# Kernel tuning notes

Hardware: AMD Instinct MI355X
Metric: run time of the kernel (lower is better)

Reference implementation:

```python
import jax, jax.numpy as jnp
import numpy as np

N, E, D, ED = 10000, 50000, 32, 16
DIMS = [(D, 8 * D), (8 * D, 16 * D), (16 * D, 16 * D), (16 * D, 16 * D)]
BI_OUT = 8 * D + ED  # 272


def _gat(h, src, dst, ea, Wl, Wr, We, att, b, n):
    """GATv2Conv, heads=1: score = att . leaky_relu(Wl x_j + Wr x_i + We e_ij); msg = Wl x_j."""
    xl = h @ Wl
    xr = h @ Wr
    ee = ea @ We
    s = jax.nn.leaky_relu(xl[src] + xr[dst] + ee, 0.2)   # [E_aug, out]
    alpha = s @ att                                       # [E_aug]
    amax = jax.lax.stop_gradient(jax.ops.segment_max(alpha, dst, num_segments=n))
    ex = jnp.exp(alpha - amax[dst])
    den = jax.ops.segment_sum(ex, dst, num_segments=n)
    w = ex / jnp.maximum(den[dst], 1e-16)
    return jax.ops.segment_sum(xl[src] * w[:, None], dst, num_segments=n) + b


def _forward(x, edge_attr, Wl0, Wr0, We0, a0, b0, Wl1, Wr1, We1, a1, b1,
             Wl2, Wr2, We2, a2, b2, Wl3, Wr3, We3, a3, b3,
             Wbi, bbi, Wm1, bm1, Wm2, bm2, Wm3, bm3, edge_index):
    src, dst = edge_index[0], edge_index[1]
    # self loops with edge_attr fill_value='mean' (mean of incoming edge_attr per target node)
    cnt = jax.ops.segment_sum(jnp.ones((E,), jnp.float32), dst, num_segments=N)
    mean_attr = jax.ops.segment_sum(edge_attr, dst, num_segments=N) / jnp.maximum(cnt, 1.0)[:, None]
    loop = jnp.arange(N, dtype=edge_index.dtype)
    src_a = jnp.concatenate([src, loop])
    dst_a = jnp.concatenate([dst, loop])
    ea_a = jnp.concatenate([edge_attr, mean_attr], axis=0)

    h = x
    layers = [(Wl0, Wr0, We0, a0, b0), (Wl1, Wr1, We1, a1, b1),
              (Wl2, Wr2, We2, a2, b2), (Wl3, Wr3, We3, a3, b3)]
    for i, (Wl, Wr, We, a, b) in enumerate(layers):
        h = _gat(h, src_a, dst_a, ea_a, Wl, Wr, We, a, b, N)
        if i < 3:
            h = jax.nn.relu(h)

    # edge scoring: gather both endpoints, bilinear with edge_attr, then MLP -> sigmoid
    z = jnp.concatenate([h[src], h[dst]], axis=1)           # [E, 2*16*D] = [E, 1024]
    bi = jnp.einsum('ni,kij,nj->nk', z, Wbi, edge_attr) + bbi  # [E, 272]
    m = jax.nn.relu(bi @ Wm1 + bm1)
    m = jax.nn.relu(m @ Wm2 + bm2)
    return jax.nn.sigmoid(m @ Wm3 + bm3)                    # [E, 1]


def setup_inputs() -> dict:
    ki = iter(jax.random.split(jax.random.key(0), 40))

    def rn(shape, s=0.05):
        return jax.random.normal(next(ki), shape, dtype=jnp.float32) * s

    inp = {
        "x": rn((N, D), 1.0),
        "edge_attr": rn((E, ED), 1.0),
        "edge_index": jax.random.randint(next(ki), (2, E), 0, N, dtype=jnp.int32),
    }
    for i, (din, dout) in enumerate(DIMS):
        inp[f"Wl{i}"] = rn((din, dout))
        inp[f"Wr{i}"] = rn((din, dout))
        inp[f"We{i}"] = rn((ED, dout))
        inp[f"a{i}"] = rn((dout,))
        inp[f"b{i}"] = jnp.zeros((dout,), jnp.float32)
    inp["Wbi"] = rn((BI_OUT, 2 * 16 * D, ED), 0.02)
    inp["bbi"] = jnp.zeros((BI_OUT,), jnp.float32)
    inp["Wm1"] = rn((BI_OUT, BI_OUT))
    inp["bm1"] = jnp.zeros((BI_OUT,), jnp.float32)
    inp["Wm2"] = rn((BI_OUT, D))
    inp["bm2"] = jnp.zeros((D,), jnp.float32)
    inp["Wm3"] = rn((D, 1))
    inp["bm3"] = jnp.zeros((1,), jnp.float32)
    return inp


def reference(x, edge_attr, edge_index, Wl0, Wr0, We0, a0, b0, Wl1, Wr1, We1, a1, b1,
              Wl2, Wr2, We2, a2, b2, Wl3, Wr3, We3, a3, b3,
              Wbi, bbi, Wm1, bm1, Wm2, bm2, Wm3, bm3):
    return _forward(x, edge_attr, Wl0, Wr0, We0, a0, b0, Wl1, Wr1, We1, a1, b1,
                    Wl2, Wr2, We2, a2, b2, Wl3, Wr3, We3, a3, b3,
                    Wbi, bbi, Wm1, bm1, Wm2, bm2, Wm3, bm3, edge_index)
```

## Files before the change

### kernel.cpp

```cpp
#include <hip/hip_runtime.h>
#include <hip/hip_bf16.h>
#include <hip/hip_fp16.h>
#include <cstdio>

#define N_NODES 10000
#define M_NODEP 10240
#define N_EDGES 50000
#define M_EDGEP 50176
#define E_AUG   60000
#define E_AUGP  60160
#define ED      16
#define BI_OUT  272
#define KP      288

typedef __attribute__((ext_vector_type(8))) short s16x8;
typedef __attribute__((ext_vector_type(4))) short s16x4;
typedef __attribute__((ext_vector_type(8))) _Float16 h16x8;
typedef __attribute__((ext_vector_type(4))) _Float16 h16x4;
typedef __attribute__((ext_vector_type(4))) float f32x4;

__device__ inline void stc(float* p, float v){ *p = v; }
__device__ inline void stc(__hip_bfloat16* p, float v){ *p = __float2bfloat16(v); }
__device__ inline void stc(__half* p, float v){ *p = __float2half(v); }
__device__ inline float bf2f(short s){ return __uint_as_float(((unsigned)(unsigned short)s) << 16); }
__device__ inline short f2bf(float f){ __hip_bfloat16 h = __float2bfloat16(f); return *(short*)&h; }

__device__ __forceinline__ void gl2lds16(const void* g, void* l){
  __builtin_amdgcn_global_load_lds((const __attribute__((address_space(1))) void*)g,
                                   (__attribute__((address_space(3))) void*)l, 16, 0, 0);
}

__global__ void edge_attr_sum_k(const float* __restrict__ ea, const int* __restrict__ ei,
                                float* __restrict__ meanat, float* __restrict__ cntF){
  int t = blockIdx.x*256 + threadIdx.x;
  if (t >= N_EDGES*ED) return;
  int e = t >> 4, j = t & 15;
  int dst = ei[N_EDGES + e];
  atomicAdd(&meanat[dst*ED + j], ea[t]);
  if (j == 0) atomicAdd(&cntF[dst], 1.0f);
}

__global__ void mean_div_k(float* __restrict__ meanat, const float* __restrict__ cntF){
  int t = blockIdx.x*256 + threadIdx.x;
  if (t >= N_NODES*ED) return;
  meanat[t] /= fmaxf(cntF[t>>4], 1.0f);
}

__global__ void scan_k(const float* __restrict__ cntF, int* __restrict__ rowptr){
  __shared__ int s[1024];
  int tid = threadIdx.x;
  int loc[10]; int sum = 0;
  #pragma unroll
  for (int k = 0; k < 10; ++k){
    int i = tid*10 + k;
    int v = (i < N_NODES) ? ((int)cntF[i] + 1) : 0;
    loc[k] = sum; sum += v;
  }
  s[tid] = sum; __syncthreads();
  for (int off = 1; off < 1024; off <<= 1){
    int t2 = (tid >= off) ? s[tid-off] : 0;
    __syncthreads();
    s[tid] += t2;
    __syncthreads();
  }
  int pre = s[tid] - sum;
  #pragma unroll
  for (int k = 0; k < 10; ++k){
    int i = tid*10 + k;
    if (i < N_NODES) rowptr[i] = pre + loc[k];
  }
  if (tid == 1023) rowptr[N_NODES] = s[1023];
}

__global__ void scatter_k(const int* __restrict__ ei, const int* __restrict__ rowptr,
                          int* __restrict__ fill, int* __restrict__ csr){
  int e = blockIdx.x*256 + threadIdx.x;
  if (e >= E_AUG) return;
  int dst = (e < N_EDGES) ? ei[N_EDGES+e] : (e - N_EDGES);
  int pos = rowptr[dst] + atomicAdd(&fill[dst], 1);
  csr[pos] = e;
}

template<typename TC, bool BIAS, bool RELU>
__global__ __launch_bounds__(256)
void mfma_gemm_k(const __hip_bfloat16* __restrict__ A, const __hip_bfloat16* __restrict__ Bt,
                 TC* __restrict__ C, const float* __restrict__ bias,
                 int Mstore, int K, int lda, int ldb, int ldc){
  __shared__ __align__(16) __hip_bfloat16 Asm[4096];
  __shared__ __align__(16) __hip_bfloat16 Bsm[4096];
  const int tid = threadIdx.x;
  const int lane = tid & 63, wave = tid >> 6;
  const int wm = (wave >> 1) * 64, wn = (wave & 1) * 64;
  const int m0 = blockIdx.x * 128, n0 = blockIdx.y * 128;
  const int quad = lane >> 4, r16 = lane & 15;

  f32x4 acc[4][4];
  #pragma unroll
  for (int i = 0; i < 4; ++i)
    #pragma unroll
    for (int j = 0; j < 4; ++j)
      acc[i][j] = (f32x4){0.f, 0.f, 0.f, 0.f};

  const int rl = lane >> 2, cq = lane & 3;
  const int row0 = wave*32 + rl;
  const int qg = (cq - ((row0 >> 1) & 3)) & 3;
  const __hip_bfloat16* ga0 = &A[(size_t)(m0 + row0)*lda + qg*8];
  const __hip_bfloat16* ga1 = &A[(size_t)(m0 + row0 + 16)*lda + qg*8];
  const __hip_bfloat16* gb0 = &Bt[(size_t)(n0 + row0)*ldb + qg*8];
  const __hip_bfloat16* gb1 = &Bt[(size_t)(n0 + row0 + 16)*ldb + qg*8];
  __hip_bfloat16* lA0 = &Asm[(wave*32)*32];
  __hip_bfloat16* lA1 = &Asm[(wave*32 + 16)*32];
  __hip_bfloat16* lB0 = &Bsm[(wave*32)*32];
  __hip_bfloat16* lB1 = &Bsm[(wave*32 + 16)*32];

  for (int k0 = 0; k0 < K; k0 += 32){
    gl2lds16(ga0 + k0, lA0);
    gl2lds16(ga1 + k0, lA1);
    gl2lds16(gb0 + k0, lB0);
    gl2lds16(gb1 + k0, lB1);
    __syncthreads();
    s16x8 af[4], bf[4];
    #pragma unroll
    for (int i = 0; i < 4; ++i){
      int row = wm + i*16 + r16;
      af[i] = *(const s16x8*)&Asm[row*32 + (((quad + (row >> 1)) & 3) << 3)];
    }
    #pragma unroll
    for (int j = 0; j < 4; ++j){
      int row = wn + j*16 + r16;
      bf[j] = *(const s16x8*)&Bsm[row*32 + (((quad + (row >> 1)) & 3) << 3)];
    }
    #pragma unroll
    for (int i = 0; i < 4; ++i)
      #pragma unroll
      for (int j = 0; j < 4; ++j)
        acc[i][j] = __builtin_amdgcn_mfma_f32_16x16x32_bf16(af[i], bf[j], acc[i][j], 0, 0, 0);
    __syncthreads();
  }
  #pragma unroll
  for (int i = 0; i < 4; ++i){
    #pragma unroll
    for (int reg = 0; reg < 4; ++reg){
      int gr = m0 + wm + i*16 + quad*4 + reg;
      if (gr >= Mstore) continue;
      #pragma unroll
      for (int j = 0; j < 4; ++j){
        int gc = n0 + wn + j*16 + r16;
        float v = acc[i][j][reg];
        if (BIAS) v += bias[gc];
        if (RELU) v = fmaxf(v, 0.f);
        stc(&C[(size_t)gr*ldc + gc], v);
      }
    }
  }
}

__global__ void prep_weights_k(
    const float* __restrict__ Wl0, const float* __restrict__ Wr0, const float* __restrict__ We0,
    const float* __restrict__ Wl1, const float* __restrict__ Wr1, const float* __restrict__ We1,
    const float* __restrict__ Wl2, const float* __restrict__ Wr2, const float* __restrict__ We2,
    const float* __restrict__ Wl3, const float* __restrict__ Wr3, const float* __restrict__ We3,
    const float* __restrict__ Wm1, const float* __restrict__ bm1,
    const float* __restrict__ Wm2, const float* __restrict__ bm2,
    __hip_bfloat16* __restrict__ WTa, __hip_bfloat16* __restrict__ WeTa,
    __hip_bfloat16* __restrict__ Wm1T, __hip_bfloat16* __restrict__ Wm2T,
    float* __restrict__ bm1p, float* __restrict__ bm2p){
  int t = blockIdx.x*256 + threadIdx.x;
  if (t < 16384){
    int half = t >> 13, r = t & 8191, i = r >> 8, j = r & 255;
    WTa[(half*256 + j)*32 + i] = __float2bfloat16(half ? Wr0[r] : Wl0[r]);
  } else if (t < 278528){
    int u = t - 16384, half = u >> 17, r = u & 131071, i = r >> 9, j = r & 511;
    WTa[16384 + (half*512 + j)*256 + i] = __float2bfloat16(half ? Wr1[r] : Wl1[r]);
  } else if (t < 802816){
    int u = t - 278528, half = u >> 18, r = u & 262143, i = r >> 9, j = r & 511;
    WTa[278528 + (half*512 + j)*512 + i] = __float2bfloat16(half ? Wr2[r] : Wl2[r]);
  } else if (t < 1327104){
    int u = t - 802816, half = u >> 18, r = u & 262143, i = r >> 9, j = r & 511;
    WTa[802816 + (half*512 + j)*512 + i] = __float2bfloat16(half ? Wr3[r] : Wl3[r]);
  }
  if (t < 8192){
    int n = t >> 5, k = t & 31;
    WeTa[t] = __float2bfloat16((k < 16) ? We0[k*256 + n] : 0.f);
  } else if (t < 24576){
    int u = t - 8192, n = u >> 5, k = u & 31;
    WeTa[t] = __float2bfloat16((k < 16) ? We1[k*512 + n] : 0.f);
  } else if (t < 40960){
    int u = t - 24576, n = u >> 5, k = u & 31;
    WeTa[t] = __float2bfloat16((k < 16) ? We2[k*512 + n] : 0.f);
  } else if (t < 57344){
    int u = t - 40960, n = u >> 5, k = u & 31;
    WeTa[t] = __float2bfloat16((k < 16) ? We3[k*512 + n] : 0.f);
  }
  if (t < 384*KP){
    int n = t / KP, k = t - n*KP;
    Wm1T[t] = __float2bfloat16((n < BI_OUT && k < BI_OUT) ? Wm1[(size_t)k*BI_OUT + n] : 0.f);
  }
  if (t < 128*KP){
    int n = t / KP, k = t - n*KP;
    Wm2T[t] = __float2bfloat16((n < 32 && k < BI_OUT) ? Wm2[(size_t)k*32 + n] : 0.f);
  }
  if (t < 384) bm1p[t] = (t < BI_OUT) ? bm1[t] : 0.f;
  if (t < 128) bm2p[t] = (t < 32) ? bm2[t] : 0.f;
}

__global__ void cast_h_k(const float* __restrict__ h, __hip_bfloat16* __restrict__ hb, int K){
  int t = blockIdx.x*256 + threadIdx.x;
  if (t >= M_NODEP*K) return;
  int r = t / K;
  hb[t] = (r < N_NODES) ? __float2bfloat16(h[t]) : __float2bfloat16(0.f);
}

__global__ void cast_ea_k(const float* __restrict__ ea, const float* __restrict__ meanat,
                          __hip_bfloat16* __restrict__ eab){
  int t = blockIdx.x*256 + threadIdx.x;
  if (t >= E_AUGP*32) return;
  int e = t >> 5, j = t & 31;
  float v = 0.f;
  if (j < 16){
    if (e < N_EDGES) v = ea[(size_t)e*ED + j];
    else if (e < E_AUG) v = meanat[(size_t)(e - N_EDGES)*ED + j];
  }
  eab[t] = __float2bfloat16(v);
}

__global__ void wbi_transpose_k(const float* __restrict__ Wbi, __hip_bfloat16* __restrict__ WtAll){
  int t = blockIdx.x*256 + threadIdx.x;
  if (t >= BI_OUT*1024*ED) return;
  int k = t >> 14, r = t & 16383;
  int i = r >> 4, j = r & 15;
  int c = (k < 96) ? 0 : ((k < 192) ? 1 : 2);
  int kb = c*96;
  int base = c*3072;
  int cw = (c < 2) ? 1536 : 1280;
  int row = base + ((i >= 512) ? cw : 0) + (k - kb)*16 + j;
  WtAll[(size_t)row*512 + (i & 511)] = __float2bfloat16(Wbi[t]);
}

template<int DOUT, bool RELU>
__global__ __launch_bounds__(256)
void gat_fused_k(const __hip_bfloat16* __restrict__ XLXR, const __half* __restrict__ EE,
                 const int* __restrict__ ei, const int* __restrict__ rowptr,
                 const int* __restrict__ csr, const float* __restrict__ att,
                 const float* __restrict__ b, __hip_bfloat16* __restrict__ hb){
  constexpr int NI = DOUT/64;
  constexpr int W2 = 2*DOUT;
  int wave = threadIdx.x >> 6, lane = threadIdx.x & 63;
  int n = blockIdx.x*4 + wave;
  if (n >= N_NODES) return;
  int r0 = rowptr[n], r1 = rowptr[n+1];
  int pp = r0 + lane;
  int e_l = 0, s_l = 0;
  if (pp < r1){
    e_l = csr[pp];
    s_l = (e_l < N_EDGES) ? ei[e_l] : (e_l - N_EDGES);
  }
  float xr[NI], at[NI], acc[NI];
  #pragma unroll
  for (int i = 0; i < NI; ++i){
    int d = lane*NI + i;
    xr[i]  = bf2f(((const short*)XLXR)[(size_t)n*W2 + DOUT + d]);
    at[i]  = att[d];
    acc[i] = 0.f;
  }
  float mrun = -1e30f, den = 0.f;
  int p = r0;
  for (; p + 1 < r1; p += 2){
    int i0 = p - r0, i1 = i0 + 1;
    int e0, s0, e1, s1;
    if (i1 < 64){
      e0 = __shfl(e_l, i0, 64); s0 = __shfl(s_l, i0, 64);
      e1 = __shfl(e_l, i1, 64); s1 = __shfl(s_l, i1, 64);
    } else {
      if (i0 < 64){ e0 = __shfl(e_l, i0, 64); s0 = __shfl(s_l, i0, 64); }
      else { e0 = csr[p]; s0 = (e0 < N_EDGES) ? ei[e0] : (e0 - N_EDGES); }
      e1 = csr[p+1]; s1 = (e1 < N_EDGES) ? ei[e1] : (e1 - N_EDGES);
    }
    const short* xp0 = (const short*)XLXR + (size_t)s0*W2 + lane*NI;
    const short* xp1 = (const short*)XLXR + (size_t)s1*W2 + lane*NI;
    const _Float16* ep0 = (const _Float16*)EE + (size_t)e0*DOUT + lane*NI;
    const _Float16* ep1 = (const _Float16*)EE + (size_t)e1*DOUT + lane*NI;
    float xl0[NI], xl1[NI];
    float a0 = 0.f, a1 = 0.f;
    if constexpr (NI == 8){
      s16x8 xv0 = *(const s16x8*)xp0; h16x8 ev0 = *(const h16x8*)ep0;
      s16x8 xv1 = *(const s16x8*)xp1; h16x8 ev1 = *(const h16x8*)ep1;
      #pragma unroll
      for (int i = 0; i < 8; ++i){
        xl0[i] = bf2f(xv0[i]); xl1[i] = bf2f(xv1[i]);
        float v0 = xl0[i] + xr[i] + (float)ev0[i];
        float v1 = xl1[i] + xr[i] + (float)ev1[i];
        v0 = (v0 > 0.f) ? v0 : 0.2f*v0;
        v1 = (v1 > 0.f) ? v1 : 0.2f*v1;
        a0 += at[i]*v0; a1 += at[i]*v1;
      }
    } else {
      s16x4 xv0 = *(const s16x4*)xp0; h16x4 ev0 = *(const h16x4*)ep0;
      s16x4 xv1 = *(const s16x4*)xp1; h16x4 ev1 = *(const h16x4*)ep1;
      #pragma unroll
      for (int i = 0; i < 4; ++i){
        xl0[i] = bf2f(xv0[i]); xl1[i] = bf2f(xv1[i]);
        float v0 = xl0[i] + xr[i] + (float)ev0[i];
        float v1 = xl1[i] + xr[i] + (float)ev1[i];
        v0 = (v0 > 0.f) ? v0 : 0.2f*v0;
        v1 = (v1 > 0.f) ? v1 : 0.2f*v1;
        a0 += at[i]*v0; a1 += at[i]*v1;
      }
    }
    #pragma unroll
    for (int off = 32; off; off >>= 1){
      a0 += __shfl_xor(a0, off, 64);
      a1 += __shfl_xor(a1, off, 64);
    }
    float mnew = fmaxf(mrun, fmaxf(a0, a1));
    float s = __expf(mrun - mnew);
    float w0 = __expf(a0 - mnew);
    float w1 = __expf(a1 - mnew);
    den = den*s + w0 + w1;
    #pragma unroll
    for (int i = 0; i < NI; ++i) acc[i] = acc[i]*s + w0*xl0[i] + w1*xl1[i];
    mrun = mnew;
  }
  if (p < r1){
    int i0 = p - r0;
    int e0, s0;
    if (i0 < 64){ e0 = __shfl(e_l, i0, 64); s0 = __shfl(s_l, i0, 64); }
    else { e0 = csr[p]; s0 = (e0 < N_EDGES) ? ei[e0] : (e0 - N_EDGES); }
    const short* xp0 = (const short*)XLXR + (size_t)s0*W2 + lane*NI;
    const _Float16* ep0 = (const _Float16*)EE + (size_t)e0*DOUT + lane*NI;
    float xl0[NI];
    float a0 = 0.f;
    #pragma unroll
    for (int i = 0; i < NI; ++i){
      xl0[i] = bf2f(xp0[i]);
      float v0 = xl0[i] + xr[i] + (float)ep0[i];
      v0 = (v0 > 0.f) ? v0 : 0.2f*v0;
      a0 += at[i]*v0;
    }
    #pragma unroll
    for (int off = 32; off; off >>= 1) a0 += __shfl_xor(a0, off, 64);
    float mnew = fmaxf(mrun, a0);
    float s = __expf(mrun - mnew);
    float w0 = __expf(a0 - mnew);
    den = den*s + w0;
    #pragma unroll
    for (int i = 0; i < NI; ++i) acc[i] = acc[i]*s + w0*xl0[i];
    mrun = mnew;
  }
  float dinv = 1.0f / fmaxf(den, 1e-16f);
  if constexpr (NI == 8){
    s16x8 o;
    #pragma unroll
    for (int i = 0; i < 8; ++i){
      float v = b[lane*8 + i] + acc[i]*dinv;
      o[i] = f2bf(RELU ? fmaxf(v, 0.f) : v);
    }
    *(s16x8*)((short*)hb + (size_t)n*DOUT + lane*8) = o;
  } else {
    s16x4 o;
    #pragma unroll
    for (int i = 0; i < 4; ++i){
      float v = b[lane*4 + i] + acc[i]*dinv;
      o[i] = f2bf(RELU ? fmaxf(v, 0.f) : v);
    }
    *(s16x4*)((short*)hb + (size_t)n*DOUT + lane*4) = o;
  }
}

__global__ void bi_k(const __hip_bfloat16* __restrict__ P, const float* __restrict__ ea,
                     const int* __restrict__ ei, const float* __restrict__ bbi,
                     __hip_bfloat16* __restrict__ bi, int kb, int kcnt){
  int cw = kcnt*ED, w2 = 2*cw;
  int g = blockIdx.x*256 + threadIdx.x;
  if (g >= N_EDGES*kcnt) return;
  int n = g / kcnt, k = g - n*kcnt;
  int src = ei[n], dst = ei[N_EDGES+n];
  const __hip_bfloat16* pl = P + (size_t)src*w2 + k*ED;
  const __hip_bfloat16* pr = P + (size_t)dst*w2 + cw + k*ED;
  const float* eap = ea + (size_t)n*ED;
  float s = 0.f;
  #pragma unroll
  for (int j = 0; j < ED; ++j)
    s += eap[j]*(__bfloat162float(pl[j]) + __bfloat162float(pr[j]));
  int kg = kb + k;
  bi[(size_t)n*KP + kg] = __float2bfloat16(s + bbi[kg]);
}

__global__ void out_k(const __hip_bfloat16* __restrict__ m2, const float* __restrict__ Wm3,
                      const float* __restrict__ bm3, float* __restrict__ out){
  int n = blockIdx.x*256 + threadIdx.x;
  if (n >= N_EDGES) return;
  float acc = bm3[0];
  #pragma unroll
  for (int j = 0; j < 32; ++j) acc += __bfloat162float(m2[(size_t)n*128 + j])*Wm3[j];
  out[n] = 1.0f/(1.0f + __expf(-acc));
}

extern "C" void kernel_launch(void* const* d_in, const int* in_sizes, int n_in,
                              void* d_out, int out_size, void* d_ws, size_t ws_size,
                              hipStream_t stream) {
  const float* x   = (const float*)d_in[0];
  const float* ea  = (const float*)d_in[1];
  const int*   ei  = (const int*)d_in[2];
  const float* Wl[4]  = {(const float*)d_in[3],(const float*)d_in[8],(const float*)d_in[13],(const float*)d_in[18]};
  const float* Wr[4]  = {(const float*)d_in[4],(const float*)d_in[9],(const float*)d_in[14],(const float*)d_in[19]};
  const float* We[4]  = {(const float*)d_in[5],(const float*)d_in[10],(const float*)d_in[15],(const float*)d_in[20]};
  const float* att[4] = {(const float*)d_in[6],(const float*)d_in[11],(const float*)d_in[16],(const float*)d_in[21]};
  const float* bia[4] = {(const float*)d_in[7],(const float*)d_in[12],(const float*)d_in[17],(const float*)d_in[22]};
  const float* Wbi = (const float*)d_in[23];
  const float* bbi = (const float*)d_in[24];
  const float* Wm1 = (const float*)d_in[25];
  const float* bm1 = (const float*)d_in[26];
  const float* Wm2 = (const float*)d_in[27];
  const float* bm2 = (const float*)d_in[28];
  const float* Wm3 = (const float*)d_in[29];
  const float* bm3 = (const float*)d_in[30];
  float* out = (float*)d_out;

  char* ws = (char*)d_ws;
  size_t off = 0;
  auto alloc = [&](size_t b){ off = (off + 255) & ~(size_t)255; size_t o = off; off += b; return o; };
  size_t o_bi   = alloc((size_t)M_EDGEP*KP*2);
  size_t o_XLXR = alloc((size_t)M_NODEP*1024*2);
  size_t o_hb   = alloc((size_t)M_NODEP*512*2);
  size_t o_eab  = alloc((size_t)E_AUGP*32*2);
  size_t o_WTa  = alloc((size_t)1327104*2);
  size_t o_WeTa = alloc((size_t)57344*2);
  size_t o_WtA  = alloc((size_t)8704*512*2);
  size_t o_EEP  = alloc((size_t)63000000);
  size_t o_Wm1T = alloc((size_t)384*KP*2);
  size_t o_Wm2T = alloc((size_t)128*KP*2);
  size_t o_bm1p = alloc(384*4);
  size_t o_bm2p = alloc(128*4);
  size_t o_ma   = alloc((size_t)N_NODES*ED*4);
  size_t o_cnt  = alloc(40000);
  size_t o_rp   = alloc(40004);
  size_t o_fill = alloc(40000);
  size_t o_csr  = alloc(240000);
  if (off > ws_size){
    fprintf(stderr, "kernel_launch: workspace too small: need %zu have %zu\n", off, ws_size);
    return;
  }

  float* meanat = (float*)(ws + o_ma);
  float* cntF   = (float*)(ws + o_cnt);
  int*   rowptr = (int*)(ws + o_rp);
  int*   fill   = (int*)(ws + o_fill);
  int*   csr    = (int*)(ws + o_csr);
  __hip_bfloat16* XLXR = (__hip_bfloat16*)(ws + o_XLXR);
  __hip_bfloat16* hb   = (__hip_bfloat16*)(ws + o_hb);
  __hip_bfloat16* eab  = (__hip_bfloat16*)(ws + o_eab);
  __hip_bfloat16* WTa  = (__hip_bfloat16*)(ws + o_WTa);
  __hip_bfloat16* WeTa = (__hip_bfloat16*)(ws + o_WeTa);
  __hip_bfloat16* WtA  = (__hip_bfloat16*)(ws + o_WtA);
  __half*        EE    = (__half*)(ws + o_EEP);
  __hip_bfloat16* P    = (__hip_bfloat16*)(ws + o_EEP);
  __hip_bfloat16* Wm1T = (__hip_bfloat16*)(ws + o_Wm1T);
  __hip_bfloat16* Wm2T = (__hip_bfloat16*)(ws + o_Wm2T);
  float* bm1p = (float*)(ws + o_bm1p);
  float* bm2p = (float*)(ws + o_bm2p);
  __hip_bfloat16* bi = (__hip_bfloat16*)(ws + o_bi);
  __hip_bfloat16* m1 = (__hip_bfloat16*)(ws + o_EEP);
  __hip_bfloat16* m2 = (__hip_bfloat16*)(ws + o_EEP + 40000000);

  hipMemsetAsync(ws + o_ma, 0, (o_cnt - o_ma) + 40000, stream);
  hipMemsetAsync(ws + o_fill, 0, 40000, stream);
  edge_attr_sum_k<<<3125, 256, 0, stream>>>(ea, ei, meanat, cntF);
  mean_div_k<<<625, 256, 0, stream>>>(meanat, cntF);
  scan_k<<<1, 1024, 0, stream>>>(cntF, rowptr);
  scatter_k<<<235, 256, 0, stream>>>(ei, rowptr, fill, csr);

  cast_h_k<<<(M_NODEP*32 + 255)/256, 256, 0, stream>>>(x, hb, 32);
  cast_ea_k<<<(E_AUGP*32 + 255)/256, 256, 0, stream>>>(ea, meanat, eab);
  prep_weights_k<<<5184, 256, 0, stream>>>(
      Wl[0], Wr[0], We[0], Wl[1], Wr[1], We[1], Wl[2], Wr[2], We[2], Wl[3], Wr[3], We[3],
      Wm1, bm1, Wm2, bm2, WTa, WeTa, Wm1T, Wm2T, bm1p, bm2p);
  wbi_transpose_k<<<(BI_OUT*1024*ED + 255)/256, 256, 0, stream>>>(Wbi, WtA);

  const int dins[4]  = {32, 256, 512, 512};
  const int douts[4] = {256, 512, 512, 512};
  const int wtOff[4] = {0, 16384, 278528, 802816};
  const int weOff[4] = {0, 8192, 24576, 40960};
  for (int L = 0; L < 4; ++L){
    int din = dins[L], dn = douts[L];
    dim3 g1(M_NODEP/128, 2*dn/128);
    mfma_gemm_k<__hip_bfloat16,false,false><<<g1, 256, 0, stream>>>(
        hb, WTa + wtOff[L], XLXR, nullptr, N_NODES, din, din, din, 2*dn);
    dim3 ge(E_AUGP/128, dn/128);
    mfma_gemm_k<__half,false,false><<<ge, 256, 0, stream>>>(
        eab, WeTa + weOff[L], EE, nullptr, E_AUG, 32, 32, 32, dn);
    if (dn == 256)
      gat_fused_k<256,true><<<2500, 256, 0, stream>>>(XLXR, EE, ei, rowptr, csr, att[L], bia[L], hb);
    else if (L == 3)
      gat_fused_k<512,false><<<2500, 256, 0, stream>>>(XLXR, EE, ei, rowptr, csr, att[L], bia[L], hb);
    else
      gat_fused_k<512,true><<<2500, 256, 0, stream>>>(XLXR, EE, ei, rowptr, csr, att[L], bia[L], hb);
  }

  const int kbs[3]   = {0, 96, 192};
  const int kcnts[3] = {96, 96, 80};
  const int bases[3] = {0, 3072, 6144};
  for (int c = 0; c < 3; ++c){
    int cw = kcnts[c]*ED, w2 = 2*cw;
    dim3 gp(M_NODEP/128, w2/128);
    mfma_gemm_k<__hip_bfloat16,false,false><<<gp, 256, 0, stream>>>(
        hb, WtA + (size_t)bases[c]*512, P, nullptr, N_NODES, 512, 512, 512, w2);
    bi_k<<<(N_EDGES*kcnts[c] + 255)/256, 256, 0, stream>>>(P, ea, ei, bbi, bi, kbs[c], kcnts[c]);
  }

  dim3 gm1(M_EDGEP/128, 3);
  mfma_gemm_k<__hip_bfloat16,true,true><<<gm1, 256, 0, stream>>>(bi, Wm1T, m1, bm1p, M_EDGEP, KP, KP, KP, 384);
  dim3 gm2(M_EDGEP/128, 1);
  mfma_gemm_k<__hip_bfloat16,true,true><<<gm2, 256, 0, stream>>>(m1, Wm2T, m2, bm2p, M_EDGEP, KP, 384, KP, 128);
  out_k<<<(N_EDGES + 255)/256, 256, 0, stream>>>(m2, Wm3, bm3, out);
}
```

Before: 695.6 us.

## Pre-swizzle GEMM B operands into MFMA fragment order and double-buffer A tiles

Weight matrices are now written during prep into a blocked layout matching the MFMA B-fragment order, so each wave loads its B fragments straight from global memory into registers instead of staging them through LDS. The A tile gets a two-stage LDS double buffer, and the next step's B fragments are prefetched into registers, which removes one barrier per k-step. The aim is to cut LDS traffic and sync overhead in all the GEMMs. The cost is higher register pressure and uncoalesced-looking per-wave B loads that depend on L2 hits.

```diff
diff --git a/kernel.cpp b/kernel.cpp
--- a/kernel.cpp
+++ b/kernel.cpp
@@ -30,6 +30,12 @@
                                    (__attribute__((address_space(3))) void*)l, 16, 0, 0);
 }
 
+__device__ inline size_t preidx(int n, int k, int kSteps){
+  int nb = n >> 7, f = (n >> 4) & 7, r = n & 15;
+  int s = k >> 5, q = (k >> 3) & 3, ii = k & 7;
+  return ((((size_t)nb*kSteps + s)*8 + f)*64 + q*16 + r)*8 + ii;
+}
+
 __global__ void edge_attr_sum_k(const float* __restrict__ ea, const int* __restrict__ ei,
                                 float* __restrict__ meanat, float* __restrict__ cntF){
   int t = blockIdx.x*256 + threadIdx.x;
@@ -83,16 +89,16 @@
 
 template<typename TC, bool BIAS, bool RELU>
 __global__ __launch_bounds__(256)
-void mfma_gemm_k(const __hip_bfloat16* __restrict__ A, const __hip_bfloat16* __restrict__ Bt,
+void mfma_gemm_k(const __hip_bfloat16* __restrict__ A, const __hip_bfloat16* __restrict__ Bp,
                  TC* __restrict__ C, const float* __restrict__ bias,
-                 int Mstore, int K, int lda, int ldb, int ldc){
-  __shared__ __align__(16) __hip_bfloat16 Asm[4096];
-  __shared__ __align__(16) __hip_bfloat16 Bsm[4096];
+                 int Mstore, int K, int lda, int ldc){
+  __shared__ __align__(16) __hip_bfloat16 Asm[2][4096];
   const int tid = threadIdx.x;
   const int lane = tid & 63, wave = tid >> 6;
   const int wm = (wave >> 1) * 64, wn = (wave & 1) * 64;
   const int m0 = blockIdx.x * 128, n0 = blockIdx.y * 128;
   const int quad = lane >> 4, r16 = lane & 15;
+  const int kSteps = K >> 5;
 
   f32x4 acc[4][4];
   #pragma unroll
@@ -106,36 +112,39 @@
   const int qg = (cq - ((row0 >> 1) & 3)) & 3;
   const __hip_bfloat16* ga0 = &A[(size_t)(m0 + row0)*lda + qg*8];
   const __hip_bfloat16* ga1 = &A[(size_t)(m0 + row0 + 16)*lda + qg*8];
-  const __hip_bfloat16* gb0 = &Bt[(size_t)(n0 + row0)*ldb + qg*8];
-  const __hip_bfloat16* gb1 = &Bt[(size_t)(n0 + row0 + 16)*ldb + qg*8];
-  __hip_bfloat16* lA0 = &Asm[(wave*32)*32];
-  __hip_bfloat16* lA1 = &Asm[(wave*32 + 16)*32];
-  __hip_bfloat16* lB0 = &Bsm[(wave*32)*32];
-  __hip_bfloat16* lB1 = &Bsm[(wave*32 + 16)*32];
-
-  for (int k0 = 0; k0 < K; k0 += 32){
-    gl2lds16(ga0 + k0, lA0);
-    gl2lds16(ga1 + k0, lA1);
-    gl2lds16(gb0 + k0, lB0);
-    gl2lds16(gb1 + k0, lB1);
+  const int aoff0 = (wave*32)*32, aoff1 = (wave*32 + 16)*32;
+
+  const __hip_bfloat16* gB = Bp + (((size_t)blockIdx.y*kSteps)*8 + (wn >> 4))*512 + (size_t)lane*8;
+
+  gl2lds16(ga0, &Asm[0][aoff0]);
+  gl2lds16(ga1, &Asm[0][aoff1]);
+  s16x8 bcur[4], bnxt[4];
+  #pragma unroll
+  for (int j = 0; j < 4; ++j) bcur[j] = *(const s16x8*)(gB + j*512);
+
+  for (int s = 0; s < kSteps; ++s){
     __syncthreads();
-    s16x8 af[4], bf[4];
+    if (s + 1 < kSteps){
+      int k0 = (s + 1) * 32;
+      gl2lds16(ga0 + k0, &Asm[(s+1)&1][aoff0]);
+      gl2lds16(ga1 + k0, &Asm[(s+1)&1][aoff1]);
+      const __hip_bfloat16* gBn = gB + (size_t)(s+1)*4096;
+      #pragma unroll
+      for (int j = 0; j < 4; ++j) bnxt[j] = *(const s16x8*)(gBn + j*512);
+    }
+    s16x8 af[4];
     #pragma unroll
     for (int i = 0; i < 4; ++i){
       int row = wm + i*16 + r16;
-      af[i] = *(const s16x8*)&Asm[row*32 + (((quad + (row >> 1)) & 3) << 3)];
-    }
-    #pragma unroll
-    for (int j = 0; j < 4; ++j){
-      int row = wn + j*16 + r16;
-      bf[j] = *(const s16x8*)&Bsm[row*32 + (((quad + (row >> 1)) & 3) << 3)];
+      af[i] = *(const s16x8*)&Asm[s & 1][row*32 + (((quad + (row >> 1)) & 3) << 3)];
     }
     #pragma unroll
     for (int i = 0; i < 4; ++i)
       #pragma unroll
       for (int j = 0; j < 4; ++j)
-        acc[i][j] = __builtin_amdgcn_mfma_f32_16x16x32_bf16(af[i], bf[j], acc[i][j], 0, 0, 0);
-    __syncthreads();
+        acc[i][j] = __builtin_amdgcn_mfma_f32_16x16x32_bf16(af[i], bcur[j], acc[i][j], 0, 0, 0);
+    #pragma unroll
+    for (int j = 0; j < 4; ++j) bcur[j] = bnxt[j];
   }
   #pragma unroll
   for (int i = 0; i < 4; ++i){
@@ -168,37 +177,37 @@
   int t = blockIdx.x*256 + threadIdx.x;
   if (t < 16384){
     int half = t >> 13, r = t & 8191, i = r >> 8, j = r & 255;
-    WTa[(half*256 + j)*32 + i] = __float2bfloat16(half ? Wr0[r] : Wl0[r]);
+    WTa[preidx(half*256 + j, i, 1)] = __float2bfloat16(half ? Wr0[r] : Wl0[r]);
   } else if (t < 278528){
     int u = t - 16384, half = u >> 17, r = u & 131071, i = r >> 9, j = r & 511;
-    WTa[16384 + (half*512 + j)*256 + i] = __float2bfloat16(half ? Wr1[r] : Wl1[r]);
+    WTa[16384 + preidx(half*512 + j, i, 8)] = __float2bfloat16(half ? Wr1[r] : Wl1[r]);
   } else if (t < 802816){
     int u = t - 278528, half = u >> 18, r = u & 262143, i = r >> 9, j = r & 511;
-    WTa[278528 + (half*512 + j)*512 + i] = __float2bfloat16(half ? Wr2[r] : Wl2[r]);
+    WTa[278528 + preidx(half*512 + j, i, 16)] = __float2bfloat16(half ? Wr2[r] : Wl2[r]);
   } else if (t < 1327104){
     int u = t - 802816, half = u >> 18, r = u & 262143, i = r >> 9, j = r & 511;
-    WTa[802816 + (half*512 + j)*512 + i] = __float2bfloat16(half ? Wr3[r] : Wl3[r]);
+    WTa[802816 + preidx(half*512 + j, i, 16)] = __float2bfloat16(half ? Wr3[r] : Wl3[r]);
   }
   if (t < 8192){
     int n = t >> 5, k = t & 31;
-    WeTa[t] = __float2bfloat16((k < 16) ? We0[k*256 + n] : 0.f);
+    WeTa[preidx(n, k, 1)] = __float2bfloat16((k < 16) ? We0[k*256 + n] : 0.f);
   } else if (t < 24576){
     int u = t - 8192, n = u >> 5, k = u & 31;
-    WeTa[t] = __float2bfloat16((k < 16) ? We1[k*512 + n] : 0.f);
+    WeTa[8192 + preidx(n, k, 1)] = __float2bfloat16((k < 16) ? We1[k*512 + n] : 0.f);
   } else if (t < 40960){
     int u = t - 24576, n = u >> 5, k = u & 31;
-    WeTa[t] = __float2bfloat16((k < 16) ? We2[k*512 + n] : 0.f);
+    WeTa[24576 + preidx(n, k, 1)] = __float2bfloat16((k < 16) ? We2[k*512 + n] : 0.f);
   } else if (t < 57344){
     int u = t - 40960, n = u >> 5, k = u & 31;
-    WeTa[t] = __float2bfloat16((k < 16) ? We3[k*512 + n] : 0.f);
+    WeTa[40960 + preidx(n, k, 1)] = __float2bfloat16((k < 16) ? We3[k*512 + n] : 0.f);
   }
   if (t < 384*KP){
     int n = t / KP, k = t - n*KP;
-    Wm1T[t] = __float2bfloat16((n < BI_OUT && k < BI_OUT) ? Wm1[(size_t)k*BI_OUT + n] : 0.f);
+    Wm1T[preidx(n, k, 9)] = __float2bfloat16((n < BI_OUT && k < BI_OUT) ? Wm1[(size_t)k*BI_OUT + n] : 0.f);
   }
   if (t < 128*KP){
     int n = t / KP, k = t - n*KP;
-    Wm2T[t] = __float2bfloat16((n < 32 && k < BI_OUT) ? Wm2[(size_t)k*32 + n] : 0.f);
+    Wm2T[preidx(n, k, 9)] = __float2bfloat16((n < 32 && k < BI_OUT) ? Wm2[(size_t)k*32 + n] : 0.f);
   }
   if (t < 384) bm1p[t] = (t < BI_OUT) ? bm1[t] : 0.f;
   if (t < 128) bm2p[t] = (t < 32) ? bm2[t] : 0.f;
@@ -231,10 +240,10 @@
   int i = r >> 4, j = r & 15;
   int c = (k < 96) ? 0 : ((k < 192) ? 1 : 2);
   int kb = c*96;
-  int base = c*3072;
   int cw = (c < 2) ? 1536 : 1280;
-  int row = base + ((i >= 512) ? cw : 0) + (k - kb)*16 + j;
-  WtAll[(size_t)row*512 + (i & 511)] = __float2bfloat16(Wbi[t]);
+  size_t baseE = (size_t)c * 1572864;
+  int row = ((i >= 512) ? cw : 0) + (k - kb)*16 + j;
+  WtAll[baseE + preidx(row, i & 511, 16)] = __float2bfloat16(Wbi[t]);
 }
 
 template<int DOUT, bool RELU>
@@ -485,10 +494,10 @@
     int din = dins[L], dn = douts[L];
     dim3 g1(M_NODEP/128, 2*dn/128);
     mfma_gemm_k<__hip_bfloat16,false,false><<<g1, 256, 0, stream>>>(
-        hb, WTa + wtOff[L], XLXR, nullptr, N_NODES, din, din, din, 2*dn);
+        hb, WTa + wtOff[L], XLXR, nullptr, N_NODES, din, din, 2*dn);
     dim3 ge(E_AUGP/128, dn/128);
     mfma_gemm_k<__half,false,false><<<ge, 256, 0, stream>>>(
-        eab, WeTa + weOff[L], EE, nullptr, E_AUG, 32, 32, 32, dn);
+        eab, WeTa + weOff[L], EE, nullptr, E_AUG, 32, 32, dn);
     if (dn == 256)
       gat_fused_k<256,true><<<2500, 256, 0, stream>>>(XLXR, EE, ei, rowptr, csr, att[L], bia[L], hb);
     else if (L == 3)
@@ -497,20 +506,20 @@
       gat_fused_k<512,true><<<2500, 256, 0, stream>>>(XLXR, EE, ei, rowptr, csr, att[L], bia[L], hb);
   }
 
-  const int kbs[3]   = {0, 96, 192};
-  const int kcnts[3] = {96, 96, 80};
-  const int bases[3] = {0, 3072, 6144};
+  const int kbs[3]      = {0, 96, 192};
+  const int kcnts[3]    = {96, 96, 80};
+  const size_t baseE[3] = {0, 1572864, 3145728};
   for (int c = 0; c < 3; ++c){
     int cw = kcnts[c]*ED, w2 = 2*cw;
     dim3 gp(M_NODEP/128, w2/128);
     mfma_gemm_k<__hip_bfloat16,false,false><<<gp, 256, 0, stream>>>(
-        hb, WtA + (size_t)bases[c]*512, P, nullptr, N_NODES, 512, 512, 512, w2);
+        hb, WtA + baseE[c], P, nullptr, N_NODES, 512, 512, w2);
     bi_k<<<(N_EDGES*kcnts[c] + 255)/256, 256, 0, stream>>>(P, ea, ei, bbi, bi, kbs[c], kcnts[c]);
   }
 
   dim3 gm1(M_EDGEP/128, 3);
-  mfma_gemm_k<__hip_bfloat16,true,true><<<gm1, 256, 0, stream>>>(bi, Wm1T, m1, bm1p, M_EDGEP, KP, KP, KP, 384);
+  mfma_gemm_k<__hip_bfloat16,true,true><<<gm1, 256, 0, stream>>>(bi, Wm1T, m1, bm1p, M_EDGEP, KP, KP, 384);
   dim3 gm2(M_EDGEP/128, 1);
-  mfma_gemm_k<__hip_bfloat16,true,true><<<gm2, 256, 0, stream>>>(m1, Wm2T, m2, bm2p, M_EDGEP, KP, 384, KP, 128);
+  mfma_gemm_k<__hip_bfloat16,true,true><<<gm2, 256, 0, stream>>>(m1, Wm2T, m2, bm2p, M_EDGEP, KP, 384, 128);
   out_k<<<(N_EDGES + 255)/256, 256, 0, stream>>>(m2, Wm3, bm3, out);
 }
```

Result: faster. 657.8 us (-5.4%).
